# Kernel tuning notes

Measured on AMD Instinct MI355X. Metric: run time of the kernel, lower is better.

The kernel has to match this reference:

```python
import jax, jax.numpy as jnp
import numpy as np

N_NODES = 50000
N_EDGES = 800000
IN_DIM = 128
HID = 32
HEADS = 8
N_CLASSES = 10
N_GRAPHS = 64
NEG_SLOPE = 0.2


def _lin(key, fan_in, fan_out):
    return jax.random.normal(key, (fan_in, fan_out), jnp.float32) / np.sqrt(fan_in)


def setup_inputs() -> dict:
    key = jax.random.key(0)
    ks = jax.random.split(key, 24)
    x = jax.random.normal(ks[0], (N_NODES, IN_DIM), jnp.float32)
    edge_index = jax.random.randint(ks[1], (2, N_EDGES), 0, N_NODES, jnp.int64)
    batch = jnp.sort(jax.random.randint(ks[2], (N_NODES,), 0, N_GRAPHS, jnp.int64))
    HC = HEADS * HID
    return {
        "x": x,
        "edge_index": edge_index,
        "batch": batch,
        # GATConv(IN_DIM, HID, heads=8): shared lin, att_src/att_dst, bias on concat output
        "gat_W": _lin(ks[3], IN_DIM, HC),
        "gat_att_src": jax.random.normal(ks[4], (HEADS, HID), jnp.float32) / np.sqrt(HID),
        "gat_att_dst": jax.random.normal(ks[5], (HEADS, HID), jnp.float32) / np.sqrt(HID),
        "gat_b": jnp.zeros((HC,), jnp.float32),
        # GraphConv(HC, HID): lin_rel (bias) on aggregated neighbors + lin_root (no bias)
        "W2_rel": _lin(ks[6], HC, HID), "b2": jnp.zeros((HID,), jnp.float32), "W2_root": _lin(ks[7], HC, HID),
        # SAGEConv(HID, HID): lin_l (bias) on mean-aggregated neighbors + lin_r (no bias)
        "W3_l": _lin(ks[8], HID, HID), "b3": jnp.zeros((HID,), jnp.float32), "W3_r": _lin(ks[9], HID, HID),
        # GraphConv(HID, HID)
        "W4_rel": _lin(ks[10], HID, HID), "b4": jnp.zeros((HID,), jnp.float32), "W4_root": _lin(ks[11], HID, HID),
        "fc1_W": _lin(ks[12], HID, HID), "fc1_b": jnp.zeros((HID,), jnp.float32),
        "fc2_W": _lin(ks[13], HID, N_CLASSES), "fc2_b": jnp.zeros((N_CLASSES,), jnp.float32),
    }


def _segment_softmax(logits, seg_ids, num_segments):
    # numerically-stable softmax over edges grouped by destination node
    m = jax.ops.segment_max(logits, seg_ids, num_segments=num_segments)
    e = jnp.exp(logits - m[seg_ids])
    z = jax.ops.segment_sum(e, seg_ids, num_segments=num_segments)
    return e / (z[seg_ids] + 1e-16)


def _gnn_forward(x, edge_index, batch, gat_W, gat_att_src, gat_att_dst, gat_b,
                 W2_rel, b2, W2_root, W3_l, b3, W3_r, W4_rel, b4, W4_root,
                 fc1_W, fc1_b, fc2_W, fc2_b):
    N = x.shape[0]
    src0, dst0 = edge_index[0], edge_index[1]

    # ---- GATConv (PyG defaults: add_self_loops=True, concat heads, neg_slope=0.2) ----
    loops = jnp.arange(N)
    src = jnp.concatenate([src0, loops])
    dst = jnp.concatenate([dst0, loops])
    h = (x @ gat_W).reshape(N, HEADS, HID)                 # [N,H,C]
    a_src = jnp.sum(h * gat_att_src, axis=-1)              # [N,H]
    a_dst = jnp.sum(h * gat_att_dst, axis=-1)              # [N,H]
    logits = jax.nn.leaky_relu(a_src[src] + a_dst[dst], NEG_SLOPE)  # [E',H]
    alpha = _segment_softmax(logits, dst, N)               # [E',H]
    msg = h[src] * alpha[:, :, None]                       # [E',H,C]
    out = jax.ops.segment_sum(msg, dst, num_segments=N).reshape(N, HEADS * HID) + gat_b
    x1 = jax.nn.relu(out)

    # ---- GraphConv (aggr='add'): lin_rel(sum_j x_j) + lin_root(x) ----
    agg = jax.ops.segment_sum(x1[src0], dst0, num_segments=N)
    x2 = jax.nn.relu(agg @ W2_rel + b2 + x1 @ W2_root)

    # ---- SAGEConv (aggr='mean'): lin_l(mean_j x_j) + lin_r(x) ----
    deg = jax.ops.segment_sum(jnp.ones((src0.shape[0],), x2.dtype), dst0, num_segments=N)
    agg = jax.ops.segment_sum(x2[src0], dst0, num_segments=N) / jnp.clip(deg, 1.0)[:, None]
    x3 = jax.nn.relu(agg @ W3_l + b3 + x2 @ W3_r)

    # ---- GraphConv ----
    agg = jax.ops.segment_sum(x3[src0], dst0, num_segments=N)
    x4 = jax.nn.relu(agg @ W4_rel + b4 + x3 @ W4_root)

    # ---- global_mean_pool + MLP head ----
    gsum = jax.ops.segment_sum(x4, batch, num_segments=N_GRAPHS)
    gcnt = jax.ops.segment_sum(jnp.ones((N,), x4.dtype), batch, num_segments=N_GRAPHS)
    g = gsum / jnp.clip(gcnt, 1.0)[:, None]                # [G,HID]
    g = jax.nn.relu(g @ fc1_W + fc1_b)
    return g @ fc2_W + fc2_b                               # [G, N_CLASSES]


def reference(x, edge_index, batch, gat_W, gat_att_src, gat_att_dst, gat_b,
              W2_rel, b2, W2_root, W3_l, b3, W3_r, W4_rel, b4, W4_root,
              fc1_W, fc1_b, fc2_W, fc2_b):
    return _gnn_forward(x, edge_index, batch, gat_W, gat_att_src, gat_att_dst, gat_b,
                        W2_rel, b2, W2_root, W3_l, b3, W3_r, W4_rel, b4, W4_root,
                        fc1_W, fc1_b, fc2_W, fc2_b)
```

## Files before the change

### kernel.cpp

```cpp
#include <hip/hip_runtime.h>

#define IN_DIM 128
#define HID 32
#define HEADS 8
#define HC 256
#define N_GRAPHS 64
#define N_CLASSES 10

#define SCAN_ELEMS 8
#define SCAN_BLOCK 256
#define SCAN_CHUNK (SCAN_ELEMS * SCAN_BLOCK)

typedef __attribute__((ext_vector_type(8))) short bf16x8;
typedef __attribute__((ext_vector_type(4))) float f32x4;

__device__ __forceinline__ float leaky(float v) { return v > 0.f ? v : 0.2f * v; }

__device__ __forceinline__ unsigned fenc(float f) {
    unsigned u = __float_as_uint(f);
    return (u & 0x80000000u) ? ~u : (u | 0x80000000u);
}
__device__ __forceinline__ float fdec(unsigned u) {
    return __uint_as_float((u & 0x80000000u) ? (u & 0x7FFFFFFFu) : ~u);
}
__device__ __forceinline__ unsigned short bf16r(float f) {
    unsigned u = __float_as_uint(f);
    return (unsigned short)((u + 0x7FFFu + ((u >> 16) & 1u)) >> 16);
}
__device__ __forceinline__ float bdec(unsigned short u) {
    return __uint_as_float(((unsigned)u) << 16);
}

__global__ __launch_bounds__(256) void k_setup(
    int* __restrict__ deg, int N, unsigned* __restrict__ gm,
    float* __restrict__ gsum, float* __restrict__ gcnt, int* __restrict__ counter,
    const float* __restrict__ W, const float* __restrict__ Wrel, const float* __restrict__ Wroot,
    unsigned short* __restrict__ Wb, unsigned short* __restrict__ W2b)
{
    int i = blockIdx.x * 256 + threadIdx.x;
    if (i < N) deg[i] = 0;
    if (i < HEADS) gm[i] = 0u;
    if (i < N_GRAPHS * HID) gsum[i] = 0.f;
    if (i < N_GRAPHS) gcnt[i] = 0.f;
    if (i == 0) *counter = 0;

    if (blockIdx.x < 16) {
        int slot = blockIdx.x * 256 + threadIdx.x;
        int lane = slot & 63;
        int ctg  = (slot >> 6) & 15;
        int ks   = slot >> 10;
        int col  = ctg * 16 + (lane & 15);
        int kb   = ks * 32 + (lane >> 4) * 8;
        unsigned short t[8];
#pragma unroll
        for (int j = 0; j < 8; ++j) t[j] = bf16r(W[(size_t)(kb + j) * HC + col]);
        ushort4* dst = (ushort4*)(Wb + (size_t)slot * 8);
        dst[0] = make_ushort4(t[0], t[1], t[2], t[3]);
        dst[1] = make_ushort4(t[4], t[5], t[6], t[7]);
    } else if (blockIdx.x < 24) {
        int slot = (blockIdx.x - 16) * 256 + threadIdx.x;
        int lane = slot & 63;
        int ct   = (slot >> 6) & 3;
        int ks   = slot >> 8;
        int col  = ct * 16 + (lane & 15);
        int kb   = ks * 32 + (lane >> 4) * 8;
        const float* src = (col < HID) ? (Wrel + col) : (Wroot + (col - HID));
        unsigned short t[8];
#pragma unroll
        for (int j = 0; j < 8; ++j) t[j] = bf16r(src[(size_t)(kb + j) * HID]);
        ushort4* dst = (ushort4*)(W2b + (size_t)slot * 8);
        dst[0] = make_ushort4(t[0], t[1], t[2], t[3]);
        dst[1] = make_ushort4(t[4], t[5], t[6], t[7]);
    }
}

__global__ __launch_bounds__(256) void k_gemm_deg(
    const float* __restrict__ x, const unsigned short* __restrict__ Wb,
    const float* __restrict__ att_s, const float* __restrict__ att_d,
    unsigned short* __restrict__ h, float* __restrict__ a_src, float* __restrict__ a_dst, int N,
    const int* __restrict__ edst, int* __restrict__ deg, unsigned short* __restrict__ rank,
    int E, int gemmBlocks)
{
    __shared__ unsigned short sh[4][16][72];
    if (blockIdx.x >= gemmBlocks) {
        int i = (blockIdx.x - gemmBlocks) * 256 + threadIdx.x;
        if (i < E) rank[i] = (unsigned short)atomicAdd(&deg[edst[i]], 1);
        return;
    }
    int w = threadIdx.x >> 6;
    int lane = threadIdx.x & 63;
    int lrow = lane & 15, lgrp = lane >> 4;
    int nb = blockIdx.x * 16;

    int rowc = min(nb + lrow, N - 1);
    const float* xrow = x + (size_t)rowc * IN_DIM + lgrp * 8;

    f32x4 acc0 = {0.f, 0.f, 0.f, 0.f}, acc1 = acc0, acc2 = acc0, acc3 = acc0;

#pragma unroll
    for (int ks = 0; ks < 4; ++ks) {
        float4 a0 = *(const float4*)(xrow + ks * 32);
        float4 a1 = *(const float4*)(xrow + ks * 32 + 4);
        bf16x8 af;
        af[0] = (short)bf16r(a0.x); af[1] = (short)bf16r(a0.y);
        af[2] = (short)bf16r(a0.z); af[3] = (short)bf16r(a0.w);
        af[4] = (short)bf16r(a1.x); af[5] = (short)bf16r(a1.y);
        af[6] = (short)bf16r(a1.z); af[7] = (short)bf16r(a1.w);
        const bf16x8* bp = (const bf16x8*)(Wb + ((size_t)(ks * 16 + w * 4) * 64 + lane) * 8);
        acc0 = __builtin_amdgcn_mfma_f32_16x16x32_bf16(af, bp[0 * 64], acc0, 0, 0, 0);
        acc1 = __builtin_amdgcn_mfma_f32_16x16x32_bf16(af, bp[1 * 64], acc1, 0, 0, 0);
        acc2 = __builtin_amdgcn_mfma_f32_16x16x32_bf16(af, bp[2 * 64], acc2, 0, 0, 0);
        acc3 = __builtin_amdgcn_mfma_f32_16x16x32_bf16(af, bp[3 * 64], acc3, 0, 0, 0);
    }

    int cbase = w * 64;
#pragma unroll
    for (int r = 0; r < 4; ++r) {
        int lr = lgrp * 4 + r;
        sh[w][lr][lrow]      = bf16r(acc0[r]);
        sh[w][lr][16 + lrow] = bf16r(acc1[r]);
        sh[w][lr][32 + lrow] = bf16r(acc2[r]);
        sh[w][lr][48 + lrow] = bf16r(acc3[r]);
    }
#pragma unroll
    for (int round = 0; round < 2; ++round) {
        int row = (lane >> 3) + round * 8;
        int chunk = lane & 7;
        int n = nb + row;
        if (n < N) {
            uint4 t = *(const uint4*)(&sh[w][row][chunk * 8]);
            *(uint4*)(h + (size_t)n * HC + cbase + chunk * 8) = t;
        }
    }
    int h0 = cbase >> 5, h1 = h0 + 1;
    float as00 = att_s[h0 * HID + lrow], as01 = att_s[h0 * HID + 16 + lrow];
    float as10 = att_s[h1 * HID + lrow], as11 = att_s[h1 * HID + 16 + lrow];
    float ad00 = att_d[h0 * HID + lrow], ad01 = att_d[h0 * HID + 16 + lrow];
    float ad10 = att_d[h1 * HID + lrow], ad11 = att_d[h1 * HID + 16 + lrow];
#pragma unroll
    for (int r = 0; r < 4; ++r) {
        float ps0 = acc0[r] * as00 + acc1[r] * as01;
        float pd0 = acc0[r] * ad00 + acc1[r] * ad01;
        float ps1 = acc2[r] * as10 + acc3[r] * as11;
        float pd1 = acc2[r] * ad10 + acc3[r] * ad11;
#pragma unroll
        for (int d = 1; d < 16; d <<= 1) {
            ps0 += __shfl_xor(ps0, d); pd0 += __shfl_xor(pd0, d);
            ps1 += __shfl_xor(ps1, d); pd1 += __shfl_xor(pd1, d);
        }
        int n = nb + lgrp * 4 + r;
        if (lrow == 0 && n < N) {
            a_src[n * HEADS + h0] = ps0; a_dst[n * HEADS + h0] = pd0;
            a_src[n * HEADS + h1] = ps1; a_dst[n * HEADS + h1] = pd1;
        }
    }
}

__global__ __launch_bounds__(256) void k_amax_scan(
    const float* __restrict__ asrc, unsigned* __restrict__ gm, int N,
    const int* __restrict__ deg, int* __restrict__ bsum, int amaxBlocks)
{
    int tid = threadIdx.x;
    if (blockIdx.x < amaxBlocks) {
        __shared__ float sm[4][HEADS];
        float m[HEADS];
#pragma unroll
        for (int hh = 0; hh < HEADS; ++hh) m[hh] = -1e30f;
        int stride = amaxBlocks * 256;
        for (int n = blockIdx.x * 256 + tid; n < N; n += stride) {
            float4 p0 = *(const float4*)(asrc + (size_t)n * HEADS);
            float4 p1 = *(const float4*)(asrc + (size_t)n * HEADS + 4);
            m[0] = fmaxf(m[0], p0.x); m[1] = fmaxf(m[1], p0.y);
            m[2] = fmaxf(m[2], p0.z); m[3] = fmaxf(m[3], p0.w);
            m[4] = fmaxf(m[4], p1.x); m[5] = fmaxf(m[5], p1.y);
            m[6] = fmaxf(m[6], p1.z); m[7] = fmaxf(m[7], p1.w);
        }
#pragma unroll
        for (int hh = 0; hh < HEADS; ++hh)
            for (int d = 1; d < 64; d <<= 1) m[hh] = fmaxf(m[hh], __shfl_xor(m[hh], d));
        int lane = tid & 63, wv = tid >> 6;
        if (lane == 0)
#pragma unroll
            for (int hh = 0; hh < HEADS; ++hh) sm[wv][hh] = m[hh];
        __syncthreads();
        if (tid == 0) {
#pragma unroll
            for (int hh = 0; hh < HEADS; ++hh) {
                float mm = fmaxf(fmaxf(sm[0][hh], sm[1][hh]), fmaxf(sm[2][hh], sm[3][hh]));
                atomicMax(&gm[hh], fenc(mm));
            }
        }
    } else {
        int bid = blockIdx.x - amaxBlocks;
        int base = bid * SCAN_CHUNK + tid * SCAN_ELEMS;
        int s = 0;
#pragma unroll
        for (int i = 0; i < SCAN_ELEMS; ++i) { int idx = base + i; if (idx < N) s += deg[idx]; }
#pragma unroll
        for (int d = 1; d < 64; d <<= 1) s += __shfl_xor(s, d);
        __shared__ int ws[4];
        int lane = tid & 63, wv = tid >> 6;
        if (lane == 0) ws[wv] = s;
        __syncthreads();
        if (tid == 0) bsum[bid] = ws[0] + ws[1] + ws[2] + ws[3];
    }
}

__global__ __launch_bounds__(SCAN_BLOCK) void k_scan_write(
    const int* __restrict__ deg, const int* __restrict__ bsum,
    int* __restrict__ off, int N)
{
    __shared__ int sbpre;
    if (threadIdx.x < 64) {
        int lane = threadIdx.x;
        int bv = (lane < (int)blockIdx.x) ? bsum[lane] : 0;
        for (int d = 1; d < 64; d <<= 1) { int t = __shfl_up(bv, d); if (lane >= d) bv += t; }
        if (lane == 63) sbpre = bv;
    }
    int base = blockIdx.x * SCAN_CHUNK + threadIdx.x * SCAN_ELEMS;
    int dl[SCAN_ELEMS];
    int s = 0;
#pragma unroll
    for (int i = 0; i < SCAN_ELEMS; ++i) {
        int idx = base + i;
        dl[i] = (idx < N) ? deg[idx] : 0;
        s += dl[i];
    }
    int lane = threadIdx.x & 63, wv = threadIdx.x >> 6;
    int v = s;
#pragma unroll
    for (int d = 1; d < 64; d <<= 1) { int t = __shfl_up(v, d); if (lane >= d) v += t; }
    __shared__ int ws[4];
    if (lane == 63) ws[wv] = v;
    __syncthreads();
    int wadd = 0;
    for (int w = 0; w < wv; ++w) wadd += ws[w];
    int run = sbpre + wadd + (v - s);
#pragma unroll
    for (int i = 0; i < SCAN_ELEMS; ++i) {
        int idx = base + i;
        if (idx < N) {
            off[idx] = run;
            run += dl[i];
            if (idx == N - 1) off[N] = run;
        }
    }
}

__global__ void k_scatter(const int* __restrict__ src, const int* __restrict__ dst,
                          const unsigned short* __restrict__ rank, const int* __restrict__ off,
                          unsigned short* __restrict__ srcs, int E) {
    int i = blockIdx.x * blockDim.x + threadIdx.x;
    if (i < E) srcs[off[dst[i]] + (int)rank[i]] = (unsigned short)src[i];
}

__global__ __launch_bounds__(256) void k_gat(
    const unsigned short* __restrict__ h, const float* __restrict__ asrc, const float* __restrict__ adst,
    const float* __restrict__ bias, const int* __restrict__ off, const unsigned short* __restrict__ srcs,
    const unsigned* __restrict__ gm, unsigned short* __restrict__ x1, int N)
{
    int v = (blockIdx.x * blockDim.x + threadIdx.x) >> 6;
    int lane = threadIdx.x & 63;
    if (v >= N) return;
    int head = lane >> 3;
    float ad = adst[v * HEADS + head];
    float asv = asrc[v * HEADS + head];
    float m = leaky(fdec(gm[head]) + ad);
    int beg = off[v], end = off[v + 1];

    ushort4 hv = *(const ushort4*)(h + (size_t)v * HC + lane * 4);
    float w = __expf(leaky(asv + ad) - m);
    float z = w;
    float acc0 = w * bdec(hv.x), acc1 = w * bdec(hv.y), acc2 = w * bdec(hv.z), acc3 = w * bdec(hv.w);

    int e = beg;
    for (; e + 4 <= end; e += 4) {
        int s0 = srcs[e + 0], s1 = srcs[e + 1], s2 = srcs[e + 2], s3 = srcs[e + 3];
        float l0 = asrc[s0 * HEADS + head], l1 = asrc[s1 * HEADS + head];
        float l2 = asrc[s2 * HEADS + head], l3 = asrc[s3 * HEADS + head];
        ushort4 h0 = *(const ushort4*)(h + (size_t)s0 * HC + lane * 4);
        ushort4 h1 = *(const ushort4*)(h + (size_t)s1 * HC + lane * 4);
        ushort4 h2 = *(const ushort4*)(h + (size_t)s2 * HC + lane * 4);
        ushort4 h3 = *(const ushort4*)(h + (size_t)s3 * HC + lane * 4);
        float w0 = __expf(leaky(l0 + ad) - m);
        float w1 = __expf(leaky(l1 + ad) - m);
        float w2 = __expf(leaky(l2 + ad) - m);
        float w3 = __expf(leaky(l3 + ad) - m);
        z += (w0 + w1) + (w2 + w3);
        acc0 += w0 * bdec(h0.x) + w1 * bdec(h1.x) + w2 * bdec(h2.x) + w3 * bdec(h3.x);
        acc1 += w0 * bdec(h0.y) + w1 * bdec(h1.y) + w2 * bdec(h2.y) + w3 * bdec(h3.y);
        acc2 += w0 * bdec(h0.z) + w1 * bdec(h1.z) + w2 * bdec(h2.z) + w3 * bdec(h3.z);
        acc3 += w0 * bdec(h0.w) + w1 * bdec(h1.w) + w2 * bdec(h2.w) + w3 * bdec(h3.w);
    }
    for (; e < end; ++e) {
        int s = srcs[e];
        float we = __expf(leaky(asrc[s * HEADS + head] + ad) - m);
        ushort4 hs = *(const ushort4*)(h + (size_t)s * HC + lane * 4);
        z += we;
        acc0 += we * bdec(hs.x); acc1 += we * bdec(hs.y);
        acc2 += we * bdec(hs.z); acc3 += we * bdec(hs.w);
    }
    float inv_z = 1.f / (z + 1e-16f);
    int c = lane * 4;
    float4 b4 = *(const float4*)(bias + c);
    ushort4 o;
    o.x = bf16r(fmaxf(acc0 * inv_z + b4.x, 0.f));
    o.y = bf16r(fmaxf(acc1 * inv_z + b4.y, 0.f));
    o.z = bf16r(fmaxf(acc2 * inv_z + b4.z, 0.f));
    o.w = bf16r(fmaxf(acc3 * inv_z + b4.w, 0.f));
    *(ushort4*)(x1 + (size_t)v * HC + c) = o;
}

__global__ __launch_bounds__(256) void k_zr2(
    const unsigned short* __restrict__ x1b, const unsigned short* __restrict__ W2b,
    unsigned short* __restrict__ z, float* __restrict__ r, int N)
{
    int w = threadIdx.x >> 6;
    int lane = threadIdx.x & 63;
    int lrow = lane & 15, lgrp = lane >> 4;
    int nb = blockIdx.x * 16;
    int rowc = min(nb + lrow, N - 1);
    const unsigned short* xrow = x1b + (size_t)rowc * HC + lgrp * 8;

    f32x4 acc = {0.f, 0.f, 0.f, 0.f};
#pragma unroll
    for (int ks = 0; ks < 8; ++ks) {
        bf16x8 af = *(const bf16x8*)(xrow + ks * 32);
        const bf16x8* bp = (const bf16x8*)(W2b + ((size_t)(ks * 4 + w) * 64 + lane) * 8);
        acc = __builtin_amdgcn_mfma_f32_16x16x32_bf16(af, *bp, acc, 0, 0, 0);
    }
    int col = w * 16 + lrow;
#pragma unroll
    for (int rr = 0; rr < 4; ++rr) {
        int n = nb + lgrp * 4 + rr;
        if (n < N) {
            if (col < HID) z[(size_t)n * HID + col] = bf16r(acc[rr]);
            else           r[(size_t)n * HID + (col - HID)] = acc[rr];
        }
    }
}

__global__ __launch_bounds__(256) void k_agg_lin(
    const unsigned short* __restrict__ z, const float* __restrict__ r, const float* __restrict__ b,
    const int* __restrict__ off, const unsigned short* __restrict__ srcs,
    unsigned short* __restrict__ xout, int N)
{
    int nl = threadIdx.x >> 5, j = threadIdx.x & 31;
    int n = blockIdx.x * 8 + nl;
    if (n >= N) return;
    float acc = r[n * HID + j] + b[j];
    int beg = off[n], end = off[n + 1];
    int e = beg;
    for (; e + 4 <= end; e += 4) {
        int s0 = srcs[e], s1 = srcs[e + 1], s2 = srcs[e + 2], s3 = srcs[e + 3];
        float v0 = bdec(z[s0 * HID + j]);
        float v1 = bdec(z[s1 * HID + j]);
        float v2 = bdec(z[s2 * HID + j]);
        float v3 = bdec(z[s3 * HID + j]);
        acc += (v0 + v1) + (v2 + v3);
    }
    for (; e < end; ++e)
        acc += bdec(z[srcs[e] * HID + j]);
    xout[n * HID + j] = bf16r(fmaxf(acc, 0.f));
}

template <bool MEAN>
__global__ __launch_bounds__(256) void k_conv32(
    const unsigned short* __restrict__ xin, const int* __restrict__ off, const unsigned short* __restrict__ srcs,
    const float* __restrict__ Wl, const float* __restrict__ Wr, const float* __restrict__ b,
    unsigned short* __restrict__ xout, int N)
{
    __shared__ float sagg[8][HID];
    __shared__ float sx[8][HID];
    int nl = threadIdx.x >> 5, j = threadIdx.x & 31;
    int n = blockIdx.x * 8 + nl;
    int nc = min(n, N - 1);
    int beg = off[nc], end = off[nc + 1];
    float acc = 0.f;
    int e = beg;
    for (; e + 4 <= end; e += 4) {
        int s0 = srcs[e], s1 = srcs[e + 1], s2 = srcs[e + 2], s3 = srcs[e + 3];
        float v0 = bdec(xin[s0 * HID + j]);
        float v1 = bdec(xin[s1 * HID + j]);
        float v2 = bdec(xin[s2 * HID + j]);
        float v3 = bdec(xin[s3 * HID + j]);
        acc += (v0 + v1) + (v2 + v3);
    }
    for (; e < end; ++e)
        acc += bdec(xin[srcs[e] * HID + j]);
    if (MEAN) acc /= fmaxf((float)(end - beg), 1.f);
    sagg[nl][j] = acc;
    sx[nl][j] = bdec(xin[nc * HID + j]);
    __syncthreads();
    float o = b[j];
#pragma unroll
    for (int k = 0; k < HID; ++k)
        o += sagg[nl][k] * Wl[k * HID + j] + sx[nl][k] * Wr[k * HID + j];
    o = fmaxf(o, 0.f);
    if (n < N) xout[n * HID + j] = bf16r(o);
}

__global__ __launch_bounds__(256) void k_pool_head(
    const unsigned short* __restrict__ x4, const int* __restrict__ batch,
    float* __restrict__ gsum, float* __restrict__ gcnt, int N, int* __restrict__ counter,
    const float* __restrict__ fc1W, const float* __restrict__ fc1b,
    const float* __restrict__ fc2W, const float* __restrict__ fc2b,
    float* __restrict__ out)
{
    const int PER_BLOCK = 128;
    int base = blockIdx.x * PER_BLOCK;
    int endn = min(base + PER_BLOCK, N);
    int c = threadIdx.x & 31, no = threadIdx.x >> 5;
    {
        float acc = 0.f, cnt = 0.f;
        int curg = -1;
        for (int n = base + no; n < endn; n += 8) {
            int g = batch[n];
            if (g != curg) {
                if (curg >= 0) {
                    atomicAdd(&gsum[curg * HID + c], acc);
                    if (c == 0) atomicAdd(&gcnt[curg], cnt);
                }
                curg = g; acc = 0.f; cnt = 0.f;
            }
            acc += bdec(x4[n * HID + c]);
            cnt += 1.f;
        }
        if (curg >= 0) {
            atomicAdd(&gsum[curg * HID + c], acc);
            if (c == 0) atomicAdd(&gcnt[curg], cnt);
        }
    }
    __threadfence();
    __shared__ int lastFlag;
    if (threadIdx.x == 0) lastFlag = (atomicAdd(counter, 1) == (int)gridDim.x - 1);
    __syncthreads();
    if (!lastFlag) return;

    __shared__ float g[N_GRAPHS * HID];
    __shared__ float t[N_GRAPHS * HID];
    __shared__ float gc[N_GRAPHS];
    int tid = threadIdx.x;
    if (tid < N_GRAPHS) gc[tid] = atomicAdd(&gcnt[tid], 0.f);
    __syncthreads();
    for (int i = tid; i < N_GRAPHS * HID; i += 256)
        g[i] = atomicAdd(&gsum[i], 0.f) / fmaxf(gc[i >> 5], 1.f);
    __syncthreads();
    for (int i = tid; i < N_GRAPHS * HID; i += 256) {
        int gi = i >> 5, j = i & 31;
        float o = fc1b[j];
#pragma unroll
        for (int k = 0; k < HID; ++k) o += g[gi * HID + k] * fc1W[k * HID + j];
        t[i] = fmaxf(o, 0.f);
    }
    __syncthreads();
    for (int i = tid; i < N_GRAPHS * N_CLASSES; i += 256) {
        int gi = i / N_CLASSES, j = i % N_CLASSES;
        float o = fc2b[j];
#pragma unroll
        for (int k = 0; k < HID; ++k) o += t[gi * HID + k] * fc2W[k * N_CLASSES + j];
        out[i] = o;
    }
}

extern "C" void kernel_launch(void* const* d_in, const int* in_sizes, int n_in,
                              void* d_out, int out_size, void* d_ws, size_t ws_size,
                              hipStream_t stream)
{
    const float* x       = (const float*)d_in[0];
    const int*   eidx    = (const int*)d_in[1];
    const int*   batch   = (const int*)d_in[2];
    const float* gat_W   = (const float*)d_in[3];
    const float* att_s   = (const float*)d_in[4];
    const float* att_d   = (const float*)d_in[5];
    const float* gat_b   = (const float*)d_in[6];
    const float* W2_rel  = (const float*)d_in[7];
    const float* b2      = (const float*)d_in[8];
    const float* W2_root = (const float*)d_in[9];
    const float* W3_l    = (const float*)d_in[10];
    const float* b3      = (const float*)d_in[11];
    const float* W3_r    = (const float*)d_in[12];
    const float* W4_rel  = (const float*)d_in[13];
    const float* b4      = (const float*)d_in[14];
    const float* W4_root = (const float*)d_in[15];
    const float* fc1_W   = (const float*)d_in[16];
    const float* fc1_b   = (const float*)d_in[17];
    const float* fc2_W   = (const float*)d_in[18];
    const float* fc2_b   = (const float*)d_in[19];

    const int N = in_sizes[2];
    const int E = in_sizes[1] / 2;
    const int* esrc = eidx;
    const int* edst = eidx + E;

    char* wsb = (char*)d_ws;
    size_t ofs = 0;
    auto alloc = [&](size_t bytes) {
        char* p = wsb + ofs;
        ofs = (ofs + bytes + 255) & ~(size_t)255;
        return p;
    };
    unsigned short* h   = (unsigned short*)alloc((size_t)N * HC * 2);
    unsigned short* Wb  = (unsigned short*)alloc((size_t)IN_DIM * HC * 2);
    unsigned short* W2b = (unsigned short*)alloc((size_t)HC * 64 * 2);
    unsigned short* x1b = (unsigned short*)alloc((size_t)N * HC * 2);
    float* a_src = (float*)alloc((size_t)N * HEADS * 4);
    float* a_dst = (float*)alloc((size_t)N * HEADS * 4);
    int*   deg   = (int*)alloc((size_t)N * 4);
    int*   off   = (int*)alloc((size_t)(N + 1) * 4);
    unsigned short* rank = (unsigned short*)alloc((size_t)E * 2);
    unsigned short* srcs = (unsigned short*)alloc((size_t)E * 2);
    int*   bsum  = (int*)alloc((size_t)128 * 4);
    unsigned short* zb  = (unsigned short*)alloc((size_t)N * HID * 2);
    float* r     = (float*)alloc((size_t)N * HID * 4);
    unsigned short* x2b = (unsigned short*)alloc((size_t)N * HID * 2);
    unsigned short* x3b = (unsigned short*)alloc((size_t)N * HID * 2);
    unsigned short* x4b = (unsigned short*)alloc((size_t)N * HID * 2);
    float* gsum  = (float*)alloc(N_GRAPHS * HID * 4);
    float* gcnt  = (float*)alloc(N_GRAPHS * 4);
    unsigned* gm = (unsigned*)alloc(HEADS * 4);
    int*  counter = (int*)alloc(4);
    (void)ws_size; (void)n_in; (void)out_size;

    const int nscan = (N + SCAN_CHUNK - 1) / SCAN_CHUNK;
    const int gemmBlocks = (N + 15) / 16;
    const int degBlocks  = (E + 255) / 256;
    const int amaxBlocks = 128;
    const int poolBlocks = (N + 127) / 128;

    k_setup<<<(N + 255) / 256, 256, 0, stream>>>(deg, N, gm, gsum, gcnt, counter,
                                                 gat_W, W2_rel, W2_root, Wb, W2b);
    k_gemm_deg<<<gemmBlocks + degBlocks, 256, 0, stream>>>(
        x, Wb, att_s, att_d, h, a_src, a_dst, N, edst, deg, rank, E, gemmBlocks);
    k_amax_scan<<<amaxBlocks + nscan, 256, 0, stream>>>(a_src, gm, N, deg, bsum, amaxBlocks);
    k_scan_write<<<nscan, SCAN_BLOCK, 0, stream>>>(deg, bsum, off, N);
    k_scatter<<<(E + 255) / 256, 256, 0, stream>>>(esrc, edst, rank, off, srcs, E);
    k_gat<<<(N + 3) / 4, 256, 0, stream>>>(h, a_src, a_dst, gat_b, off, srcs, gm, x1b, N);
    k_zr2<<<(N + 15) / 16, 256, 0, stream>>>(x1b, W2b, zb, r, N);
    k_agg_lin<<<(N + 7) / 8, 256, 0, stream>>>(zb, r, b2, off, srcs, x2b, N);
    k_conv32<true><<<(N + 7) / 8, 256, 0, stream>>>(x2b, off, srcs, W3_l, W3_r, b3, x3b, N);
    k_conv32<false><<<(N + 7) / 8, 256, 0, stream>>>(x3b, off, srcs, W4_rel, W4_root, b4, x4b, N);
    k_pool_head<<<poolBlocks, 256, 0, stream>>>(x4b, batch, gsum, gcnt, N, counter,
                                                fc1_W, fc1_b, fc2_W, fc2_b, (float*)d_out);
}
```

Baseline: 303.9 us.

## Fuse GAT aggregation with GraphConv projection via shared-memory tile, split into three launches

Merges the GAT attention aggregation kernel and the following MFMA projection kernel into one. Each block aggregates 16 nodes into a shared-memory tile and then runs the bf16 MFMA projection from that tile. This removes the N×256 bf16 x1 intermediate written to and read back from global memory. The fused kernel is launched three times over node ranges, which adds launch overhead. Each block now handles four nodes per wave in sequence, so there is less parallelism per launch.

```diff
diff --git a/kernel.cpp b/kernel.cpp
--- a/kernel.cpp
+++ b/kernel.cpp
@@ -254,78 +254,75 @@
     if (i < E) srcs[off[dst[i]] + (int)rank[i]] = (unsigned short)src[i];
 }
 
-__global__ __launch_bounds__(256) void k_gat(
+__global__ __launch_bounds__(256) void k_gat_zr(
     const unsigned short* __restrict__ h, const float* __restrict__ asrc, const float* __restrict__ adst,
     const float* __restrict__ bias, const int* __restrict__ off, const unsigned short* __restrict__ srcs,
-    const unsigned* __restrict__ gm, unsigned short* __restrict__ x1, int N)
-{
-    int v = (blockIdx.x * blockDim.x + threadIdx.x) >> 6;
+    const unsigned* __restrict__ gm, const unsigned short* __restrict__ W2b,
+    unsigned short* __restrict__ z, float* __restrict__ r, int n0, int n1, int N)
+{
+    __shared__ unsigned short sx1[16][264];
+    int w = threadIdx.x >> 6;
     int lane = threadIdx.x & 63;
-    if (v >= N) return;
+    int nb = n0 + blockIdx.x * 16;
     int head = lane >> 3;
-    float ad = adst[v * HEADS + head];
-    float asv = asrc[v * HEADS + head];
-    float m = leaky(fdec(gm[head]) + ad);
-    int beg = off[v], end = off[v + 1];
-
-    ushort4 hv = *(const ushort4*)(h + (size_t)v * HC + lane * 4);
-    float w = __expf(leaky(asv + ad) - m);
-    float z = w;
-    float acc0 = w * bdec(hv.x), acc1 = w * bdec(hv.y), acc2 = w * bdec(hv.z), acc3 = w * bdec(hv.w);
-
-    int e = beg;
-    for (; e + 4 <= end; e += 4) {
-        int s0 = srcs[e + 0], s1 = srcs[e + 1], s2 = srcs[e + 2], s3 = srcs[e + 3];
-        float l0 = asrc[s0 * HEADS + head], l1 = asrc[s1 * HEADS + head];
-        float l2 = asrc[s2 * HEADS + head], l3 = asrc[s3 * HEADS + head];
-        ushort4 h0 = *(const ushort4*)(h + (size_t)s0 * HC + lane * 4);
-        ushort4 h1 = *(const ushort4*)(h + (size_t)s1 * HC + lane * 4);
-        ushort4 h2 = *(const ushort4*)(h + (size_t)s2 * HC + lane * 4);
-        ushort4 h3 = *(const ushort4*)(h + (size_t)s3 * HC + lane * 4);
-        float w0 = __expf(leaky(l0 + ad) - m);
-        float w1 = __expf(leaky(l1 + ad) - m);
-        float w2 = __expf(leaky(l2 + ad) - m);
-        float w3 = __expf(leaky(l3 + ad) - m);
-        z += (w0 + w1) + (w2 + w3);
-        acc0 += w0 * bdec(h0.x) + w1 * bdec(h1.x) + w2 * bdec(h2.x) + w3 * bdec(h3.x);
-        acc1 += w0 * bdec(h0.y) + w1 * bdec(h1.y) + w2 * bdec(h2.y) + w3 * bdec(h3.y);
-        acc2 += w0 * bdec(h0.z) + w1 * bdec(h1.z) + w2 * bdec(h2.z) + w3 * bdec(h3.z);
-        acc3 += w0 * bdec(h0.w) + w1 * bdec(h1.w) + w2 * bdec(h2.w) + w3 * bdec(h3.w);
-    }
-    for (; e < end; ++e) {
-        int s = srcs[e];
-        float we = __expf(leaky(asrc[s * HEADS + head] + ad) - m);
-        ushort4 hs = *(const ushort4*)(h + (size_t)s * HC + lane * 4);
-        z += we;
-        acc0 += we * bdec(hs.x); acc1 += we * bdec(hs.y);
-        acc2 += we * bdec(hs.z); acc3 += we * bdec(hs.w);
-    }
-    float inv_z = 1.f / (z + 1e-16f);
     int c = lane * 4;
     float4 b4 = *(const float4*)(bias + c);
-    ushort4 o;
-    o.x = bf16r(fmaxf(acc0 * inv_z + b4.x, 0.f));
-    o.y = bf16r(fmaxf(acc1 * inv_z + b4.y, 0.f));
-    o.z = bf16r(fmaxf(acc2 * inv_z + b4.z, 0.f));
-    o.w = bf16r(fmaxf(acc3 * inv_z + b4.w, 0.f));
-    *(ushort4*)(x1 + (size_t)v * HC + c) = o;
-}
-
-__global__ __launch_bounds__(256) void k_zr2(
-    const unsigned short* __restrict__ x1b, const unsigned short* __restrict__ W2b,
-    unsigned short* __restrict__ z, float* __restrict__ r, int N)
-{
-    int w = threadIdx.x >> 6;
-    int lane = threadIdx.x & 63;
+    float gmh = fdec(gm[head]);
+
+    for (int t = 0; t < 4; ++t) {
+        int v = min(nb + w * 4 + t, N - 1);
+        float ad = adst[v * HEADS + head];
+        float asv = asrc[v * HEADS + head];
+        float m = leaky(gmh + ad);
+        int beg = off[v], end = off[v + 1];
+
+        ushort4 hv = *(const ushort4*)(h + (size_t)v * HC + c);
+        float wg = __expf(leaky(asv + ad) - m);
+        float zz = wg;
+        float acc0 = wg * bdec(hv.x), acc1 = wg * bdec(hv.y), acc2 = wg * bdec(hv.z), acc3 = wg * bdec(hv.w);
+
+        int e = beg;
+        for (; e + 4 <= end; e += 4) {
+            int s0 = srcs[e + 0], s1 = srcs[e + 1], s2 = srcs[e + 2], s3 = srcs[e + 3];
+            float l0 = asrc[s0 * HEADS + head], l1 = asrc[s1 * HEADS + head];
+            float l2 = asrc[s2 * HEADS + head], l3 = asrc[s3 * HEADS + head];
+            ushort4 g0 = *(const ushort4*)(h + (size_t)s0 * HC + c);
+            ushort4 g1 = *(const ushort4*)(h + (size_t)s1 * HC + c);
+            ushort4 g2 = *(const ushort4*)(h + (size_t)s2 * HC + c);
+            ushort4 g3 = *(const ushort4*)(h + (size_t)s3 * HC + c);
+            float w0 = __expf(leaky(l0 + ad) - m);
+            float w1 = __expf(leaky(l1 + ad) - m);
+            float w2 = __expf(leaky(l2 + ad) - m);
+            float w3 = __expf(leaky(l3 + ad) - m);
+            zz += (w0 + w1) + (w2 + w3);
+            acc0 += w0 * bdec(g0.x) + w1 * bdec(g1.x) + w2 * bdec(g2.x) + w3 * bdec(g3.x);
+            acc1 += w0 * bdec(g0.y) + w1 * bdec(g1.y) + w2 * bdec(g2.y) + w3 * bdec(g3.y);
+            acc2 += w0 * bdec(g0.z) + w1 * bdec(g1.z) + w2 * bdec(g2.z) + w3 * bdec(g3.z);
+            acc3 += w0 * bdec(g0.w) + w1 * bdec(g1.w) + w2 * bdec(g2.w) + w3 * bdec(g3.w);
+        }
+        for (; e < end; ++e) {
+            int s = srcs[e];
+            float we = __expf(leaky(asrc[s * HEADS + head] + ad) - m);
+            ushort4 hs = *(const ushort4*)(h + (size_t)s * HC + c);
+            zz += we;
+            acc0 += we * bdec(hs.x); acc1 += we * bdec(hs.y);
+            acc2 += we * bdec(hs.z); acc3 += we * bdec(hs.w);
+        }
+        float inv_z = 1.f / (zz + 1e-16f);
+        ushort4 o;
+        o.x = bf16r(fmaxf(acc0 * inv_z + b4.x, 0.f));
+        o.y = bf16r(fmaxf(acc1 * inv_z + b4.y, 0.f));
+        o.z = bf16r(fmaxf(acc2 * inv_z + b4.z, 0.f));
+        o.w = bf16r(fmaxf(acc3 * inv_z + b4.w, 0.f));
+        *(ushort4*)(&sx1[w * 4 + t][c]) = o;
+    }
+    __syncthreads();
+
     int lrow = lane & 15, lgrp = lane >> 4;
-    int nb = blockIdx.x * 16;
-    int rowc = min(nb + lrow, N - 1);
-    const unsigned short* xrow = x1b + (size_t)rowc * HC + lgrp * 8;
-
     f32x4 acc = {0.f, 0.f, 0.f, 0.f};
 #pragma unroll
     for (int ks = 0; ks < 8; ++ks) {
-        bf16x8 af = *(const bf16x8*)(xrow + ks * 32);
+        bf16x8 af = *(const bf16x8*)(&sx1[lrow][ks * 32 + lgrp * 8]);
         const bf16x8* bp = (const bf16x8*)(W2b + ((size_t)(ks * 4 + w) * 64 + lane) * 8);
         acc = __builtin_amdgcn_mfma_f32_16x16x32_bf16(af, *bp, acc, 0, 0, 0);
     }
@@ -333,7 +330,7 @@
 #pragma unroll
     for (int rr = 0; rr < 4; ++rr) {
         int n = nb + lgrp * 4 + rr;
-        if (n < N) {
+        if (n < n1) {
             if (col < HID) z[(size_t)n * HID + col] = bf16r(acc[rr]);
             else           r[(size_t)n * HID + (col - HID)] = acc[rr];
         }
@@ -503,7 +500,6 @@
     unsigned short* h   = (unsigned short*)alloc((size_t)N * HC * 2);
     unsigned short* Wb  = (unsigned short*)alloc((size_t)IN_DIM * HC * 2);
     unsigned short* W2b = (unsigned short*)alloc((size_t)HC * 64 * 2);
-    unsigned short* x1b = (unsigned short*)alloc((size_t)N * HC * 2);
     float* a_src = (float*)alloc((size_t)N * HEADS * 4);
     float* a_dst = (float*)alloc((size_t)N * HEADS * 4);
     int*   deg   = (int*)alloc((size_t)N * 4);
@@ -527,6 +523,8 @@
     const int degBlocks  = (E + 255) / 256;
     const int amaxBlocks = 128;
     const int poolBlocks = (N + 127) / 128;
+    int t1 = ((N / 3 + 15) / 16) * 16;       if (t1 > N) t1 = N;
+    int t2 = ((2 * N / 3 + 15) / 16) * 16;   if (t2 > N) t2 = N;
 
     k_setup<<<(N + 255) / 256, 256, 0, stream>>>(deg, N, gm, gsum, gcnt, counter,
                                                  gat_W, W2_rel, W2_root, Wb, W2b);
@@ -535,8 +533,9 @@
     k_amax_scan<<<amaxBlocks + nscan, 256, 0, stream>>>(a_src, gm, N, deg, bsum, amaxBlocks);
     k_scan_write<<<nscan, SCAN_BLOCK, 0, stream>>>(deg, bsum, off, N);
     k_scatter<<<(E + 255) / 256, 256, 0, stream>>>(esrc, edst, rank, off, srcs, E);
-    k_gat<<<(N + 3) / 4, 256, 0, stream>>>(h, a_src, a_dst, gat_b, off, srcs, gm, x1b, N);
-    k_zr2<<<(N + 15) / 16, 256, 0, stream>>>(x1b, W2b, zb, r, N);
+    k_gat_zr<<<t1 / 16, 256, 0, stream>>>(h, a_src, a_dst, gat_b, off, srcs, gm, W2b, zb, r, 0, t1, N);
+    k_gat_zr<<<(t2 - t1) / 16, 256, 0, stream>>>(h, a_src, a_dst, gat_b, off, srcs, gm, W2b, zb, r, t1, t2, N);
+    k_gat_zr<<<(N - t2 + 15) / 16, 256, 0, stream>>>(h, a_src, a_dst, gat_b, off, srcs, gm, W2b, zb, r, t2, N, N);
     k_agg_lin<<<(N + 7) / 8, 256, 0, stream>>>(zb, r, b2, off, srcs, x2b, N);
     k_conv32<true><<<(N + 7) / 8, 256, 0, stream>>>(x2b, off, srcs, W3_l, W3_r, b3, x3b, N);
     k_conv32<false><<<(N + 7) / 8, 256, 0, stream>>>(x3b, off, srcs, W4_rel, W4_root, b4, x4b, N);
```

After: 306.2 us. No clear change (+0.8%).
